# Performance work log

Hardware: AMD Instinct MI355X
Metric: run time of the kernel (lower is better)

The kernel has to match this reference:

```python
import jax, jax.numpy as jnp
import numpy as np

# Module hyperparameters (from init_kwargs)
L = 32        # spatial length
CIN = 128     # in_channels
COUT = 256    # out_channels
N = 8         # num_filters
STRIDE = 1
K = 9         # kernel_size (l//4+1 default for l>16)


def setup_inputs() -> dict:
    key = jax.random.key(0)
    kx, kw = jax.random.split(key)
    x = jax.random.normal(kx, (32, CIN, L, L), dtype=jnp.float32)
    # weight init: uniform in [-r, r], r = sqrt(1/(cin*k*k)), shape (n, cin//8, k, k)
    r = np.sqrt(1.0 / (CIN * K * K)).astype(np.float32)
    weight = (jax.random.uniform(kw, (N, CIN // 8, K, K), dtype=jnp.float32) - 0.5) * 2.0 * r
    return {"x": x, "weight": weight}


def reference(x, weight):
    # 3D real FFT over (channel, H, W) of the input: [B, CIN, L, L//2+1] complex
    x_hat = jnp.fft.rfftn(x, axes=(1, 2, 3))
    # Zero-pad weight (cin//8 -> CIN, k -> L) and transform: [N, CIN, L, L//2+1]
    w_hat = jnp.fft.rfftn(weight, s=(CIN, L, L))
    # Broadcast multiply (no channel reduction): [B, N, CIN, L, L//2+1]
    freq_out = jnp.einsum('bchw,nchw->bnchw', x_hat, w_hat)
    # Inverse 3D real FFT over (channel, H, W): [B, N, CIN, L, L]
    out = jnp.fft.irfftn(freq_out, axes=(2, 3, 4))
    # Channel shrink: keep every shrink_ratio-th channel -> CIN/shrink = COUT/N channels
    shrink_ratio = N * CIN // COUT
    out = out[:, :, ::shrink_ratio]                       # [B, N, COUT//N, L, L]
    out = out.reshape(out.shape[0], -1, out.shape[3], out.shape[4])  # [B, COUT, L, L]
    if STRIDE == 2:
        out = out[:, :, ::2, ::2]
    return out
```

## Files before the change

### kernel.cpp

```cpp
#include <hip/hip_runtime.h>

typedef __attribute__((ext_vector_type(4)))  float f32x4;
typedef __attribute__((ext_vector_type(16))) float f32x16;
typedef __attribute__((ext_vector_type(8)))  short s16x8;

#define KK 9
#define NCHUNK 23

__device__ inline unsigned short f2bf(float f) {
    union { float f; unsigned int u; } v; v.f = f;
    unsigned int u = v.u + 0x7FFFu + ((v.u >> 16) & 1u);
    return (unsigned short)(u >> 16);
}


__global__ void prep_w32(const float* __restrict__ wgt, unsigned short* __restrict__ Bg) {
    int idx = blockIdx.x * 256 + threadIdx.x;
    if (idx >= 108 * 64 * 8) return;
    int e     = idx & 7;
    int lanei = (idx >> 3) & 63;
    int chunk = idx >> 9;
    int col   = lanei & 31;
    int khalf = lanei >> 5;
    int n  = col & 7;
    int p  = col >> 3;
    int kx = chunk / 12;
    int s  = chunk - 12 * kx;
    int ky = s - 3 + p;
    int cp = khalf * 8 + e;
    int dc = 15 - cp;
    float val = 0.f;
    if (ky >= 0 && ky <= 8)
        val = wgt[((n * 16 + dc) * KK + ky) * KK + kx];
    Bg[idx] = f2bf(val);
}

__global__ __launch_bounds__(512, 4) void fconv_mfma32(
    const float* __restrict__ x,
    const unsigned short* __restrict__ Bg,
    float* __restrict__ out)
{
    __shared__ char smb[65536];

    const int tid = threadIdx.x;
    const int b   = blockIdx.x >> 4;
    const int jp  = blockIdx.x & 15;

    const float* xb = x + ((size_t)b << 17);
    #pragma unroll
    for (int t = 0; t < 2; ++t) {
        const int j = jp + t * 16;
        int choff[16];
        #pragma unroll
        for (int i = 0; i < 16; ++i)
            choff[i] = ((4 * j - 15 + i) & 127) << 10;

        #pragma unroll
        for (int i = 0; i < 2; ++i) {
            int cell = i * 512 + tid;
            #pragma unroll
            for (int h = 0; h < 2; ++h) {
                union { unsigned short u16[8]; uint4 v; } pk;
                #pragma unroll
                for (int e = 0; e < 8; ++e)
                    pk.u16[e] = f2bf(xb[choff[h * 8 + e] + cell]);
                *(uint4*)(smb + t * 32768 + h * 16384 + cell * 16) = pk.v;
            }
        }
    }
    __syncthreads();

    const int lane  = tid & 63;
    const int wave  = tid >> 6;
    const int wrow  = lane & 31;
    const int khalf = lane >> 5;
    const int g4    = wave * 4;

    f32x16 acc0 = (f32x16)0.f;
    f32x16 acc1 = (f32x16)0.f;
    const char* bp = (const char*)Bg + (lane << 4);

    #pragma unroll 1
    for (int kx = 0; kx < 9; ++kx) {
        const int abase = (khalf << 14) + (((wrow - kx) & 31) << 4);
        const char* bpk = bp + kx * 12288;

        s16x8 bb[12];
        #pragma unroll
        for (int s = 0; s < 12; ++s)
            bb[s] = *(const s16x8*)(bpk + (s << 10));

        #pragma unroll
        for (int s = 0; s < 12; ++s) {
            int yp = (g4 + 3 - s) & 31;
            const char* ap = smb + abase + (yp << 9);
            s16x8 a0 = *(const s16x8*)(ap);
            s16x8 a1 = *(const s16x8*)(ap + 32768);
            acc0 = __builtin_amdgcn_mfma_f32_32x32x16_bf16(a0, bb[s], acc0, 0, 0, 0);
            acc1 = __builtin_amdgcn_mfma_f32_32x32x16_bf16(a1, bb[s], acc1, 0, 0, 0);
        }
    }

    const int n = wrow & 7;
    const int p = wrow >> 3;
    {
        float* ob = out + (((size_t)(b * 256 + n * 32 + jp)) << 10)
                        + ((g4 + p) << 5) + 4 * khalf;
        #pragma unroll
        for (int q = 0; q < 4; ++q) {
            f32x4 v = { acc0[4*q], acc0[4*q+1], acc0[4*q+2], acc0[4*q+3] };
            *(f32x4*)(ob + q * 8) = v;
        }
    }
    {
        float* ob = out + (((size_t)(b * 256 + n * 32 + jp + 16)) << 10)
                        + ((g4 + p) << 5) + 4 * khalf;
        #pragma unroll
        for (int q = 0; q < 4; ++q) {
            f32x4 v = { acc1[4*q], acc1[4*q+1], acc1[4*q+2], acc1[4*q+3] };
            *(f32x4*)(ob + q * 8) = v;
        }
    }
}

__global__ void prep_w(const float* __restrict__ wgt, unsigned short* __restrict__ Bg) {
    int idx = blockIdx.x * 256 + threadIdx.x;
    if (idx >= NCHUNK * 4 * 16 * 8) return;
    int e   = idx & 7;
    int col = (idx >> 3) & 15;
    int g   = (idx >> 7) & 3;
    int c   = idx >> 9;
    int pi   = g >> 1;
    int half = g & 1;
    int cp = half * 8 + e;
    int dc = 15 - cp;
    int q  = 2 * c + pi;
    int n  = col & 7;
    int t  = col >> 3;
    float val = 0.f;
    if (q <= 44) {
        int ky2 = q / 9;
        int kx  = q - 9 * ky2;
        int ky  = 2 * ky2 + t;
        if (ky <= 8)
            val = wgt[((n * 16 + dc) * KK + ky) * KK + kx];
    }
    Bg[idx] = f2bf(val);
}

__global__ __launch_bounds__(256) void fconv_mfma(
    const float* __restrict__ x,
    const unsigned short* __restrict__ Bg,
    float* __restrict__ out)
{
    __shared__ char smem[32768 + 4096];
    char*  smb     = smem;
    float* handoff = (float*)(smem + 32768);

    const int tid = threadIdx.x;
    const int b   = blockIdx.x >> 5;
    const int j   = blockIdx.x & 31;

    const float* xb = x + ((size_t)b << 17);
    int choff[16];
    #pragma unroll
    for (int i = 0; i < 16; ++i)
        choff[i] = ((4 * j - 15 + i) & 127) << 10;

    #pragma unroll
    for (int i = 0; i < 4; ++i) {
        int cell = i * 256 + tid;
        #pragma unroll
        for (int h = 0; h < 2; ++h) {
            union { unsigned short u16[8]; uint4 v; } pk;
            #pragma unroll
            for (int e = 0; e < 8; ++e)
                pk.u16[e] = f2bf(xb[choff[h * 8 + e] + cell]);
            *(uint4*)(smb + h * 16384 + cell * 16) = pk.v;
        }
    }
    __syncthreads();

    const int lane = tid & 63;
    const int wave = tid >> 6;
    const int r    = lane & 15;
    const int g    = lane >> 4;
    const int half = g & 1;
    const int pi   = g >> 1;
    const int y0   = wave * 8;

    f32x4 acc[8][2];
    #pragma unroll
    for (int dy = 0; dy < 8; ++dy) { acc[dy][0] = (f32x4)0.f; acc[dy][1] = (f32x4)0.f; }

    const char* bptr = (const char*)Bg + ((g * 16 + r) << 4);
    s16x8 bfrag = *(const s16x8*)(bptr);

    #pragma unroll 1
    for (int c = 0; c < NCHUNK; ++c) {
        int q   = 2 * c + pi;
        int ky2 = q / 9;
        int kx  = q - 9 * ky2;
        int wr  = (r - kx) & 31;
        int yb  = (y0 - 2 * ky2) & 31;
        int abase = (half << 14) + (wr << 4);

        int cn = (c < NCHUNK - 1) ? c + 1 : NCHUNK - 1;
        s16x8 bnext = *(const s16x8*)(bptr + (cn << 10));

        #pragma unroll
        for (int dy = 0; dy < 8; ++dy) {
            int yy = (yb + dy) & 31;
            int ra = abase + (yy << 9);
            s16x8 a0 = *(const s16x8*)(smb + ra);
            s16x8 a1 = *(const s16x8*)(smb + (ra ^ 256));
            acc[dy][0] = __builtin_amdgcn_mfma_f32_16x16x32_bf16(a0, bfrag, acc[dy][0], 0, 0, 0);
            acc[dy][1] = __builtin_amdgcn_mfma_f32_16x16x32_bf16(a1, bfrag, acc[dy][1], 0, 0, 0);
        }
        bfrag = bnext;
    }

    float recv[8][2][4];
    #pragma unroll
    for (int dy = 0; dy < 8; ++dy)
        #pragma unroll
        for (int h = 0; h < 2; ++h)
            #pragma unroll
            for (int i = 0; i < 4; ++i)
                recv[dy][h][i] = __shfl_xor(acc[dy][h][i], 8);

    if (r < 8) {
        #pragma unroll
        for (int h = 0; h < 2; ++h)
            *(f32x4*)&handoff[wave * 256 + r * 32 + h * 16 + g * 4] = *(f32x4*)recv[7][h];
    }
    __syncthreads();

    if (r < 8) {
        const int pw = (wave + 3) & 3;
        f32x4 prev[2];
        #pragma unroll
        for (int h = 0; h < 2; ++h)
            prev[h] = *(f32x4*)&handoff[pw * 256 + r * 32 + h * 16 + g * 4];

        float* ob = out + (((size_t)(b * 256 + r * 32 + j)) << 10) + (g << 2);
        #pragma unroll
        for (int dy = 0; dy < 8; ++dy) {
            #pragma unroll
            for (int h = 0; h < 2; ++h) {
                f32x4 t1 = (dy == 0) ? prev[h] : *(f32x4*)recv[dy - 1][h];
                f32x4 v  = acc[dy][h] + t1;
                *(f32x4*)(ob + (y0 + dy) * 32 + h * 16) = v;
            }
        }
    }
}

__global__ __launch_bounds__(256, 2) void fconv_fallback(
    const float* __restrict__ x,
    const float* __restrict__ wgt,
    float* __restrict__ out)
{
    __shared__ float sw[16 * KK * KK * 8];
    const int tid = threadIdx.x;
    for (int idx = tid; idx < 8 * 16 * KK * KK; idx += 256) {
        int n  = idx / (16 * KK * KK);
        int rm = idx - n * (16 * KK * KK);
        int dc = rm / (KK * KK);
        int r2 = rm - dc * (KK * KK);
        int ky = r2 / KK;
        int kx = r2 - ky * KK;
        sw[((dc * KK + kx) * KK + ky) * 8 + n] = wgt[idx];
    }
    __syncthreads();

    const int bid = blockIdx.x;
    const int b   = bid >> 6;
    const int j   = (bid >> 1) & 31;
    const int yh  = bid & 1;
    const int xw  = tid & 31;
    const int yg  = tid >> 5;
    const int y_base = yh * 16 + yg * 2;

    int rows[10];
    #pragma unroll
    for (int i = 0; i < 10; ++i)
        rows[i] = ((y_base + 24 + i) & 31) << 5;

    float acc[8][2];
    #pragma unroll
    for (int n = 0; n < 8; ++n) { acc[n][0] = 0.f; acc[n][1] = 0.f; }

    const int c0 = 4 * j;
    #pragma unroll 1
    for (int dc = 0; dc < 16; ++dc) {
        const int c_src = (c0 - dc) & 127;
        const float* bx = x + (((size_t)b * 128 + c_src) << 10);
        #pragma unroll 1
        for (int kx = 0; kx < KK; ++kx) {
            const int x_col = (xw - kx) & 31;
            float win[10];
            #pragma unroll
            for (int i = 0; i < 10; ++i)
                win[i] = bx[rows[i] + x_col];
            const float4* wp = (const float4*)&sw[((dc * KK + kx) * KK) * 8];
            #pragma unroll
            for (int ky = 0; ky < KK; ++ky) {
                float4 wA = wp[2 * ky];
                float4 wB = wp[2 * ky + 1];
                float x0 = win[8 - ky];
                float x1 = win[9 - ky];
                acc[0][0] += x0 * wA.x; acc[0][1] += x1 * wA.x;
                acc[1][0] += x0 * wA.y; acc[1][1] += x1 * wA.y;
                acc[2][0] += x0 * wA.z; acc[2][1] += x1 * wA.z;
                acc[3][0] += x0 * wA.w; acc[3][1] += x1 * wA.w;
                acc[4][0] += x0 * wB.x; acc[4][1] += x1 * wB.x;
                acc[5][0] += x0 * wB.y; acc[5][1] += x1 * wB.y;
                acc[6][0] += x0 * wB.z; acc[6][1] += x1 * wB.z;
                acc[7][0] += x0 * wB.w; acc[7][1] += x1 * wB.w;
            }
        }
    }
    #pragma unroll
    for (int n = 0; n < 8; ++n) {
        float* op = out + ((((size_t)b * 256) + n * 32 + j) << 10) + (y_base << 5) + xw;
        op[0]  = acc[n][0];
        op[32] = acc[n][1];
    }
}

extern "C" void kernel_launch(void* const* d_in, const int* in_sizes, int n_in,
                              void* d_out, int out_size, void* d_ws, size_t ws_size,
                              hipStream_t stream) {
    const float* x   = (const float*)d_in[0];
    const float* w   = (const float*)d_in[1];
    float*       out = (float*)d_out;

    const size_t BG32_BYTES = (size_t)108 * 64 * 8 * sizeof(unsigned short);
    const size_t BG16_BYTES = (size_t)NCHUNK * 4 * 16 * 8 * sizeof(unsigned short);

    if (ws_size >= BG32_BYTES) {
        unsigned short* Bg = (unsigned short*)d_ws;
        prep_w32<<<216, 256, 0, stream>>>(w, Bg);
        fconv_mfma32<<<512, 512, 0, stream>>>(x, Bg, out);
    } else if (ws_size >= BG16_BYTES) {
        unsigned short* Bg = (unsigned short*)d_ws;
        prep_w<<<46, 256, 0, stream>>>(w, Bg);
        fconv_mfma<<<1024, 256, 0, stream>>>(x, Bg, out);
    } else {
        fconv_fallback<<<2048, 256, 0, stream>>>(x, w, out);
    }
}
```

Before: 106.9 us.

## Reassign waves to adjacent row groups to reuse A loads and swizzle blocks

Each wave now handles one channel-group buffer and two adjacent 4-row output groups, so a single LDS A fragment feeds both accumulators across a 16-row sliding window. This replaces 24 LDS loads per kx with 16. Block indices are also remapped so that consecutive workgroups span different batches, which changes how blocks land across XCDs and caches. Each wave keeps the same MFMA count but adds some predicated loop structure.

```diff
diff --git a/kernel.cpp b/kernel.cpp
--- a/kernel.cpp
+++ b/kernel.cpp
@@ -43,8 +43,9 @@
     __shared__ char smb[65536];
 
     const int tid = threadIdx.x;
-    const int b   = blockIdx.x >> 4;
-    const int jp  = blockIdx.x & 15;
+    const int wg  = ((blockIdx.x & 7) << 6) + (blockIdx.x >> 3);
+    const int b   = wg >> 4;
+    const int jp  = wg & 15;
 
     const float* xb = x + ((size_t)b << 17);
     #pragma unroll
@@ -72,17 +73,20 @@
 
     const int lane  = tid & 63;
     const int wave  = tid >> 6;
+    const int pr    = wave & 3;
+    const int t     = wave >> 2;
     const int wrow  = lane & 31;
     const int khalf = lane >> 5;
-    const int g4    = wave * 4;
+    const int g8    = pr * 8;
 
     f32x16 acc0 = (f32x16)0.f;
     f32x16 acc1 = (f32x16)0.f;
-    const char* bp = (const char*)Bg + (lane << 4);
+    const char* bp    = (const char*)Bg + (lane << 4);
+    const char* abuf  = smb + t * 32768 + (khalf << 14);
 
     #pragma unroll 1
     for (int kx = 0; kx < 9; ++kx) {
-        const int abase = (khalf << 14) + (((wrow - kx) & 31) << 4);
+        const char* ab  = abuf + (((wrow - kx) & 31) << 4);
         const char* bpk = bp + kx * 12288;
 
         s16x8 bb[12];
@@ -91,21 +95,22 @@
             bb[s] = *(const s16x8*)(bpk + (s << 10));
 
         #pragma unroll
-        for (int s = 0; s < 12; ++s) {
-            int yp = (g4 + 3 - s) & 31;
-            const char* ap = smb + abase + (yp << 9);
-            s16x8 a0 = *(const s16x8*)(ap);
-            s16x8 a1 = *(const s16x8*)(ap + 32768);
-            acc0 = __builtin_amdgcn_mfma_f32_32x32x16_bf16(a0, bb[s], acc0, 0, 0, 0);
-            acc1 = __builtin_amdgcn_mfma_f32_32x32x16_bf16(a1, bb[s], acc1, 0, 0, 0);
-        }
-    }
-
-    const int n = wrow & 7;
-    const int p = wrow >> 3;
+        for (int rr = 0; rr < 16; ++rr) {
+            int R = (g8 - 8 + rr) & 31;
+            s16x8 a = *(const s16x8*)(ab + (R << 9));
+            if (rr <= 11)
+                acc0 = __builtin_amdgcn_mfma_f32_32x32x16_bf16(a, bb[11 - rr], acc0, 0, 0, 0);
+            if (rr >= 4)
+                acc1 = __builtin_amdgcn_mfma_f32_32x32x16_bf16(a, bb[15 - rr], acc1, 0, 0, 0);
+        }
+    }
+
+    const int n  = wrow & 7;
+    const int p  = wrow >> 3;
+    const int jj = jp + t * 16;
     {
-        float* ob = out + (((size_t)(b * 256 + n * 32 + jp)) << 10)
-                        + ((g4 + p) << 5) + 4 * khalf;
+        float* ob = out + (((size_t)(b * 256 + n * 32 + jj)) << 10)
+                        + ((g8 + p) << 5) + 4 * khalf;
         #pragma unroll
         for (int q = 0; q < 4; ++q) {
             f32x4 v = { acc0[4*q], acc0[4*q+1], acc0[4*q+2], acc0[4*q+3] };
@@ -113,8 +118,8 @@
         }
     }
     {
-        float* ob = out + (((size_t)(b * 256 + n * 32 + jp + 16)) << 10)
-                        + ((g4 + p) << 5) + 4 * khalf;
+        float* ob = out + (((size_t)(b * 256 + n * 32 + jj)) << 10)
+                        + ((g8 + 4 + p) << 5) + 4 * khalf;
         #pragma unroll
         for (int q = 0; q < 4; ++q) {
             f32x4 v = { acc1[4*q], acc1[4*q+1], acc1[4*q+2], acc1[4*q+3] };
```

Measured after the change: 110.1 us. 3.0% more time.
